# Optimization experiments

Measured on AMD Instinct MI355X. Metric: run time of the kernel, lower is better.

The kernel has to match this reference:

```python
import jax, jax.numpy as jnp
import numpy as np

B, S, D = 2, 2048, 2048
H = 16
DH = D // H  # 128, head dim for q, also the single kv head dim
ROPE_BASE = 10000.0


def _rope_cos_sin(seq_len, dim, dtype):
    inv_freq = 1.0 / (ROPE_BASE ** (jnp.arange(0, dim, 2, dtype=jnp.float32) / dim))
    t = jnp.arange(seq_len, dtype=jnp.float32)
    freqs = jnp.outer(t, inv_freq)            # [S, dim/2]
    emb = jnp.concatenate([freqs, freqs], -1)  # [S, dim]
    return jnp.cos(emb).astype(dtype), jnp.sin(emb).astype(dtype)


def _rotate_half(x):
    x1, x2 = x[..., : x.shape[-1] // 2], x[..., x.shape[-1] // 2 :]
    return jnp.concatenate([-x2, x1], axis=-1)


def setup_inputs() -> dict:
    key = jax.random.key(0)
    ks = jax.random.split(key, 7)
    s = 0.02
    return {
        "x": jax.random.normal(ks[0], (B, S, D), jnp.float32),
        "q_weight": jax.random.normal(ks[1], (H * DH, D), jnp.float32) * s,
        "q_bias": jax.random.normal(ks[2], (H * DH,), jnp.float32) * s,
        "kv_weight": jax.random.normal(ks[3], (2 * DH, D), jnp.float32) * s,
        "kv_bias": jax.random.normal(ks[4], (2 * DH,), jnp.float32) * s,
        "o_weight": jax.random.normal(ks[5], (D, H * DH), jnp.float32) * s,
        "o_bias": jax.random.normal(ks[6], (D,), jnp.float32) * s,
    }


def reference(x, q_weight, q_bias, kv_weight, kv_bias, o_weight, o_bias):
    b, s, d = x.shape
    # fused-style MQA projections (torch F.linear: y = x @ W.T + b)
    q = x @ q_weight.T + q_bias                      # [B,S,H*DH]
    kv = x @ kv_weight.T + kv_bias                   # [B,S,2*DH]
    q = q.reshape(b, s, H, DH)
    k, v = kv[..., :DH], kv[..., DH:]                # [B,S,DH] single kv head

    # rotary embedding (GPT-NeoX / rotate_half style) on q and k
    cos, sin = _rope_cos_sin(s, DH, x.dtype)         # [S,DH]
    q = q * cos[None, :, None, :] + _rotate_half(q) * sin[None, :, None, :]
    k = k * cos[None, :, :] + _rotate_half(k) * sin[None, :, :]

    # causal MQA attention (flash_attn_varlen with full masks == dense causal)
    scale = 1.0 / jnp.sqrt(jnp.asarray(DH, x.dtype))
    scores = jnp.einsum("bqhd,bkd->bhqk", q, k) * scale   # [B,H,S,S]
    causal = jnp.tril(jnp.ones((s, s), bool))
    scores = jnp.where(causal[None, None], scores, jnp.asarray(-1e9, x.dtype))
    probs = jax.nn.softmax(scores, axis=-1)
    attn = jnp.einsum("bhqk,bkd->bqhd", probs, v)         # [B,S,H,DH]

    out = attn.reshape(b, s, H * DH) @ o_weight.T + o_bias
    return out
```

## Files before the change

kernel.cpp:

```cpp
#include <hip/hip_runtime.h>
#include <math.h>

constexpr int Bb  = 2;
constexpr int Ss  = 2048;
constexpr int Dd  = 2048;
constexpr int Hh  = 16;
constexpr int DHd = 128;
constexpr int BS  = Bb * Ss;
constexpr int NQKV = 2304;

typedef __bf16 bf16x8 __attribute__((ext_vector_type(8)));
typedef float  f32x4  __attribute__((ext_vector_type(4)));

static __device__ __forceinline__ unsigned short f2bf(float f) {
  union { float f; unsigned int u; } a; a.f = f;
  unsigned int u = a.u;
  unsigned int r = (u + 0x7fffu + ((u >> 16) & 1u)) >> 16;
  return (unsigned short)r;
}
static __device__ __forceinline__ float bf2f(unsigned short u) {
  union { unsigned int u; float f; } a; a.u = ((unsigned int)u) << 16;
  return a.f;
}
static __device__ __forceinline__ int pk2bf(float lo, float hi) {
  return (int)((unsigned int)f2bf(lo) | ((unsigned int)f2bf(hi) << 16));
}
static __device__ __forceinline__ f32x4 mfma16(bf16x8 a, bf16x8 b, f32x4 c) {
  return __builtin_amdgcn_mfma_f32_16x16x32_bf16(a, b, c, 0, 0, 0);
}

__global__ __launch_bounds__(256) void cast_all(
    const float* __restrict__ qw, const float* __restrict__ kvw,
    const float* __restrict__ ow, const float* __restrict__ x,
    unsigned short* __restrict__ dst)
{
  const int i = blockIdx.x * 256 + threadIdx.x;
  const float* src; int off;
  if (i < 1048576)      { src = qw;  off = 0; }
  else if (i < 1179648) { src = kvw; off = 1048576; }
  else if (i < 2228224) { src = ow;  off = 1179648; }
  else                  { src = x;   off = 2228224; }
  const float4 v = ((const float4*)src)[i - off];
  ushort4 o;
  o.x = f2bf(v.x); o.y = f2bf(v.y); o.z = f2bf(v.z); o.w = f2bf(v.w);
  ((ushort4*)dst)[i] = o;
}

#define TM 128
#define TN 128
#define TK 32

#define GLOAD16(gp, lp)                                                        \
  __builtin_amdgcn_global_load_lds(                                            \
      (const __attribute__((address_space(1))) void*)(gp),                     \
      (__attribute__((address_space(3))) void*)(lp), 16, 0, 0)

template <bool BF16OUT>
__global__ __launch_bounds__(256) void gemm_bt_mfma(
    const unsigned short* __restrict__ A,
    const unsigned short* __restrict__ Bw,
    const float* __restrict__ bias1,
    const float* __restrict__ bias2,
    int nsplit,
    void* __restrict__ Cv,
    int M, int N, int K)
{
  __shared__ unsigned short As[TM * TK];
  __shared__ unsigned short Bs[TN * TK];

  const int tid  = threadIdx.x;
  const int w    = tid >> 6;
  const int lane = tid & 63;
  const int m0   = blockIdx.y * TM;
  const int n0   = blockIdx.x * TN;
  const int wm   = (w >> 1) * 64;
  const int wn   = (w & 1) * 64;

  f32x4 acc[4][4];
#pragma unroll
  for (int i = 0; i < 4; i++)
#pragma unroll
    for (int j = 0; j < 4; j++) acc[i][j] = (f32x4){0.f, 0.f, 0.f, 0.f};

  const int srow = lane >> 2;
  const int scol = (lane & 3) * 8;
  const unsigned short* aG0 = A  + (size_t)(m0 +      w * 16 + srow) * K + scol;
  const unsigned short* aG1 = A  + (size_t)(m0 + 64 + w * 16 + srow) * K + scol;
  const unsigned short* bG0 = Bw + (size_t)(n0 +      w * 16 + srow) * K + scol;
  const unsigned short* bG1 = Bw + (size_t)(n0 + 64 + w * 16 + srow) * K + scol;
  unsigned short* aL0 = &As[(     w * 16) * TK];
  unsigned short* aL1 = &As[(64 + w * 16) * TK];
  unsigned short* bL0 = &Bs[(     w * 16) * TK];
  unsigned short* bL1 = &Bs[(64 + w * 16) * TK];

  const int fr = lane & 15;
  const int fk = (lane >> 4) * 8;

  for (int k0 = 0; k0 < K; k0 += TK) {
    __syncthreads();
    GLOAD16(aG0 + k0, aL0);
    GLOAD16(aG1 + k0, aL1);
    GLOAD16(bG0 + k0, bL0);
    GLOAD16(bG1 + k0, bL1);
    __syncthreads();

    bf16x8 af[4], bfr[4];
#pragma unroll
    for (int i = 0; i < 4; i++)
      af[i] = *(const bf16x8*)&As[(wm + i * 16 + fr) * TK + fk];
#pragma unroll
    for (int j = 0; j < 4; j++)
      bfr[j] = *(const bf16x8*)&Bs[(wn + j * 16 + fr) * TK + fk];
#pragma unroll
    for (int i = 0; i < 4; i++)
#pragma unroll
      for (int j = 0; j < 4; j++)
        acc[i][j] = mfma16(af[i], bfr[j], acc[i][j]);
  }

  const int er = (lane >> 4) * 4;
  const int ec = lane & 15;
#pragma unroll
  for (int j = 0; j < 4; j++) {
    const int col = n0 + wn + j * 16 + ec;
    const float bv = (col < nsplit) ? bias1[col] : bias2[col - nsplit];
#pragma unroll
    for (int i = 0; i < 4; i++) {
      const int rbase = m0 + wm + i * 16 + er;
#pragma unroll
      for (int r = 0; r < 4; r++) {
        const float v = acc[i][j][r] + bv;
        if constexpr (BF16OUT)
          ((unsigned short*)Cv)[(size_t)(rbase + r) * N + col] = f2bf(v);
        else
          ((float*)Cv)[(size_t)(rbase + r) * N + col] = v;
      }
    }
  }
}

__global__ __launch_bounds__(256) void rope_q_bf16(unsigned short* __restrict__ QKV)
{
  const int row = blockIdx.x;
  const int s   = row & (Ss - 1);
  const int t   = threadIdx.x;
  const int h   = t >> 4, p = t & 15;
  unsigned short* base = QKV + (size_t)row * NQKV + h * DHd + p * 4;

  union { ushort4 v; unsigned short a[4]; } lo, hi, olo, ohi;
  lo.v = *(ushort4*)base;
  hi.v = *(ushort4*)(base + 64);
#pragma unroll
  for (int d = 0; d < 4; d++) {
    const int i = p * 4 + d;
    const float invf = exp2f(-(float)i * (13.287712379549449f / 64.0f));
    const float ang = (float)s * invf;
    const float c = cosf(ang), sn = sinf(ang);
    const float l = bf2f(lo.a[d]), hh = bf2f(hi.a[d]);
    olo.a[d] = f2bf(l * c - hh * sn);
    ohi.a[d] = f2bf(hh * c + l * sn);
  }
  *(ushort4*)base        = olo.v;
  *(ushort4*)(base + 64) = ohi.v;
}

__global__ __launch_bounds__(256) void prep_kv(
    const unsigned short* __restrict__ QKV,
    unsigned short* __restrict__ Kb,
    unsigned short* __restrict__ Vt)
{
  __shared__ unsigned short Vtile[64 * 136];

  const int blk = blockIdx.x;
  const int b   = blk >> 5;
  const int s0  = (blk & 31) * 64;
  const int t   = threadIdx.x;

  {
    const int r = t >> 2, p = t & 3;
    const int row = blk * 64 + r;
    const int s = row & (Ss - 1);
    const unsigned short* src = QKV + (size_t)row * NQKV + 2048 + p * 16;
    union { uint4 v[2]; unsigned short a[16]; } lo, hi, ol, oh;
    lo.v[0] = *(const uint4*)src;        lo.v[1] = *(const uint4*)(src + 8);
    hi.v[0] = *(const uint4*)(src + 64); hi.v[1] = *(const uint4*)(src + 72);
#pragma unroll
    for (int e = 0; e < 16; e++) {
      const int i = p * 16 + e;
      const float invf = exp2f(-(float)i * (13.287712379549449f / 64.0f));
      const float ang = (float)s * invf;
      const float c = cosf(ang), sn = sinf(ang);
      const float l = bf2f(lo.a[e]), hh = bf2f(hi.a[e]);
      ol.a[e] = f2bf(l * c - hh * sn);
      oh.a[e] = f2bf(hh * c + l * sn);
    }
    unsigned short* dst = Kb + (size_t)row * 128 + p * 16;
    *(uint4*)dst        = ol.v[0]; *(uint4*)(dst + 8)  = ol.v[1];
    *(uint4*)(dst + 64) = oh.v[0]; *(uint4*)(dst + 72) = oh.v[1];
  }

#pragma unroll
  for (int c = 0; c < 4; c++) {
    const int id = c * 256 + t;
    const int vr = id >> 4, cc = id & 15;
    *(uint4*)&Vtile[vr * 136 + cc * 8] =
        *(const uint4*)(QKV + (size_t)(blk * 64 + vr) * NQKV + 2176 + cc * 8);
  }
  __syncthreads();

  {
    const int d = t >> 1, half = t & 1;
    union { uint4 v[4]; unsigned short a[32]; } val;
#pragma unroll
    for (int kk = 0; kk < 32; kk++)
      val.a[kk] = Vtile[(half * 32 + kk) * 136 + d];
    unsigned short* dst = Vt + ((size_t)(b * 128 + d)) * Ss + s0 + half * 32;
#pragma unroll
    for (int c = 0; c < 4; c++) *(uint4*)(dst + c * 8) = val.v[c];
  }
}

__global__ __launch_bounds__(256, 4) void flash_v7(
    const unsigned short* __restrict__ QKV,
    const unsigned short* __restrict__ Kb,
    const unsigned short* __restrict__ Vt,
    unsigned short* __restrict__ attn)
{
  __shared__ unsigned short Ks[4 * 64 * 32];
  __shared__ unsigned short Vs[2 * 128 * 32];

  const int g   = (int)blockIdx.x;
  const int k4  = g >> 8;
  const int qtp = g & 31;
  const int m   = (g >> 5) & 7;
  const int hb  = m + 8 * k4;
  const int h   = hb & 15;
  const int b   = hb >> 4;
  const int q2  = (k4 & 2) ? ((qtp + 16) & 31) : qtp;
  const int qt  = (k4 & 1) ? (31 - q2) : q2;

  const int q0 = qt * 64;
  const int tid = threadIdx.x;
  const int w = tid >> 6, lane = tid & 63;
  const int lg = lane >> 4, lm = lane & 15;
  const int qrow = q0 + w * 16 + lm;
  const int qrow_hi = q0 + w * 16 + 15;

  bf16x8 qf[4];
  {
    const unsigned short* qp =
        QKV + (size_t)(b * Ss + qrow) * NQKV + h * DHd + lg * 8;
#pragma unroll
    for (int kf = 0; kf < 4; kf++) qf[kf] = *(const bf16x8*)(qp + kf * 32);
  }

  f32x4 ot[8];
#pragma unroll
  for (int dt = 0; dt < 8; dt++) ot[dt] = (f32x4){0.f, 0.f, 0.f, 0.f};
  float lsum = 0.f;

  const float sscale = 0.08838834764831845f * 1.4426950408889634f;

  const int sr  = lane >> 2;
  const int sc8 = (lane & 3) * 8;
  const unsigned short* kg =
      Kb + (size_t)b * Ss * 128 + (size_t)sr * 128 + w * 32 + sc8;
  const unsigned short* vg =
      Vt + (size_t)b * 128 * Ss + (size_t)(w * 32 + sr) * Ss + sc8;
  unsigned short* ksl  = &Ks[w * 2048];
  unsigned short* vsl0 = &Vs[(w * 32) * 32];
  unsigned short* vsl1 = &Vs[4096 + (w * 32) * 32];

  const int addr0 = (2 * (lg & 1)) * 16 + lm;
  const int addr1 = addr0 + 16;
  const bool sel_hi = (lg & 2) != 0;

  auto half32 = [&](int keybase, int tA, const unsigned short* VsP) {
    f32x4 s[2];
    s[0] = (f32x4){0.f, 0.f, 0.f, 0.f};
    s[1] = (f32x4){0.f, 0.f, 0.f, 0.f};
#pragma unroll
    for (int kf = 0; kf < 4; kf++) {
      const bf16x8 k0 = *(const bf16x8*)&Ks[kf * 2048 + ((tA)     * 16 + lm) * 32 + lg * 8];
      const bf16x8 k1 = *(const bf16x8*)&Ks[kf * 2048 + ((tA + 1) * 16 + lm) * 32 + lg * 8];
      s[0] = mfma16(k0, qf[kf], s[0]);
      s[1] = mfma16(k1, qf[kf], s[1]);
    }
    int pk[2][2];
#pragma unroll
    for (int t = 0; t < 2; t++) {
      float p[4];
#pragma unroll
      for (int r = 0; r < 4; r++) {
        const int key = keybase + t * 16 + 4 * lg + r;
        const float ev = exp2f(s[t][r] * sscale);
        p[r] = (key <= qrow) ? ev : 0.f;
        lsum += p[r];
      }
      pk[t][0] = pk2bf(p[0], p[1]);
      pk[t][1] = pk2bf(p[2], p[3]);
    }
    union { int d[4]; bf16x8 v; } pb;
#pragma unroll
    for (int d = 0; d < 4; d++) {
      const int src = (d < 2) ? addr0 : addr1;
      const int v0 = __shfl(pk[0][d & 1], src);
      const int v1 = __shfl(pk[1][d & 1], src);
      pb.d[d] = sel_hi ? v1 : v0;
    }
#pragma unroll
    for (int dt = 0; dt < 8; dt++) {
      const bf16x8 vfrag = *(const bf16x8*)&VsP[(dt * 16 + lm) * 32 + lg * 8];
      ot[dt] = mfma16(vfrag, pb.v, ot[dt]);
    }
  };

  for (int j0 = 0; j0 <= q0; j0 += 64) {
    __syncthreads();
#pragma unroll
    for (int i = 0; i < 4; i++)
      GLOAD16(kg + (size_t)(j0 + i * 16) * 128, ksl + i * 512);
#pragma unroll
    for (int i = 0; i < 2; i++) {
      GLOAD16(vg + (size_t)(i * 16) * Ss + j0,      vsl0 + i * 512);
      GLOAD16(vg + (size_t)(i * 16) * Ss + j0 + 32, vsl1 + i * 512);
    }
    __syncthreads();

    half32(j0, 0, &Vs[0]);
    if (j0 + 32 <= qrow_hi)
      half32(j0 + 32, 2, &Vs[4096]);
  }

  lsum += __shfl_xor(lsum, 16);
  lsum += __shfl_xor(lsum, 32);
  const float inv = 1.0f / lsum;

  unsigned short* dst = attn + (size_t)(b * Ss + qrow) * Dd + h * DHd + lg * 4;
#pragma unroll
  for (int dt = 0; dt < 8; dt++) {
    ushort4 o4;
    o4.x = f2bf(ot[dt][0] * inv);
    o4.y = f2bf(ot[dt][1] * inv);
    o4.z = f2bf(ot[dt][2] * inv);
    o4.w = f2bf(ot[dt][3] * inv);
    *(ushort4*)(dst + dt * 16) = o4;
  }
}

extern "C" void kernel_launch(void* const* d_in, const int* in_sizes, int n_in,
                              void* d_out, int out_size, void* d_ws, size_t ws_size,
                              hipStream_t stream) {
  const float* x   = (const float*)d_in[0];
  const float* qw  = (const float*)d_in[1];
  const float* qb  = (const float*)d_in[2];
  const float* kvw = (const float*)d_in[3];
  const float* kvb = (const float*)d_in[4];
  const float* ow  = (const float*)d_in[5];
  const float* ob  = (const float*)d_in[6];
  float* out = (float*)d_out;

  unsigned short* wsb    = (unsigned short*)d_ws;
  unsigned short* wqkv   = wsb;
  unsigned short* owb    = wsb + 4718592;
  unsigned short* xb     = wsb + 8912896;
  unsigned short* attn_b = xb;
  unsigned short* QKV    = wsb + 17301504;
  unsigned short* Kb     = wsb + 26738688;
  unsigned short* Vt     = wsb + 27262976;

  cast_all<<<16896, 256, 0, stream>>>(qw, kvw, ow, x, wqkv);

  gemm_bt_mfma<true><<<dim3(NQKV / TN, BS / TM), 256, 0, stream>>>(
      xb, wqkv, qb, kvb, 2048, QKV, BS, NQKV, Dd);

  rope_q_bf16<<<BS, 256, 0, stream>>>(QKV);
  prep_kv<<<BS / 64, 256, 0, stream>>>(QKV, Kb, Vt);

  flash_v7<<<1024, 256, 0, stream>>>(QKV, Kb, Vt, attn_b);

  gemm_bt_mfma<false><<<dim3(Dd / TN, BS / TM), 256, 0, stream>>>(
      attn_b, owb, ob, ob, Dd, out, BS, Dd, Dd);
}
```

Before: 324.4 us.

## Fuse Q rotary embedding into flash kernel and XOR-swizzle K/V LDS layout

Removes the standalone rope_q_bf16 kernel and applies the rotary embedding to Q inside the flash attention kernel while its fragments are loaded into registers. This saves one kernel launch and a full read-write pass over the Q portion of the QKV buffer. It also XOR-swizzles the 16-byte chunk position used for the K and V shared-memory stores and reads, aiming to cut LDS bank conflicts. In exchange each flash block recomputes the sin and cos values for its Q rows, which adds transcendental work and register pressure.

```diff
diff --git a/kernel.cpp b/kernel.cpp
--- a/kernel.cpp
+++ b/kernel.cpp
@@ -139,31 +139,6 @@
   }
 }
 
-__global__ __launch_bounds__(256) void rope_q_bf16(unsigned short* __restrict__ QKV)
-{
-  const int row = blockIdx.x;
-  const int s   = row & (Ss - 1);
-  const int t   = threadIdx.x;
-  const int h   = t >> 4, p = t & 15;
-  unsigned short* base = QKV + (size_t)row * NQKV + h * DHd + p * 4;
-
-  union { ushort4 v; unsigned short a[4]; } lo, hi, olo, ohi;
-  lo.v = *(ushort4*)base;
-  hi.v = *(ushort4*)(base + 64);
-#pragma unroll
-  for (int d = 0; d < 4; d++) {
-    const int i = p * 4 + d;
-    const float invf = exp2f(-(float)i * (13.287712379549449f / 64.0f));
-    const float ang = (float)s * invf;
-    const float c = cosf(ang), sn = sinf(ang);
-    const float l = bf2f(lo.a[d]), hh = bf2f(hi.a[d]);
-    olo.a[d] = f2bf(l * c - hh * sn);
-    ohi.a[d] = f2bf(hh * c + l * sn);
-  }
-  *(ushort4*)base        = olo.v;
-  *(ushort4*)(base + 64) = ohi.v;
-}
-
 __global__ __launch_bounds__(256) void prep_kv(
     const unsigned short* __restrict__ QKV,
     unsigned short* __restrict__ Kb,
@@ -220,7 +195,7 @@
   }
 }
 
-__global__ __launch_bounds__(256, 4) void flash_v7(
+__global__ __launch_bounds__(256, 4) void flash_v8(
     const unsigned short* __restrict__ QKV,
     const unsigned short* __restrict__ Kb,
     const unsigned short* __restrict__ Vt,
@@ -246,12 +221,41 @@
   const int qrow = q0 + w * 16 + lm;
   const int qrow_hi = q0 + w * 16 + 15;
 
+  const int klg = lg ^ ((lm >> 1) & 3);
+
   bf16x8 qf[4];
   {
     const unsigned short* qp =
         QKV + (size_t)(b * Ss + qrow) * NQKV + h * DHd + lg * 8;
-#pragma unroll
-    for (int kf = 0; kf < 4; kf++) qf[kf] = *(const bf16x8*)(qp + kf * 32);
+    union U8 { bf16x8 v; unsigned short a[8]; };
+    U8 lo0, lo1, hi0, hi1, ol0, ol1, oh0, oh1;
+    lo0.v = *(const bf16x8*)(qp);
+    lo1.v = *(const bf16x8*)(qp + 32);
+    hi0.v = *(const bf16x8*)(qp + 64);
+    hi1.v = *(const bf16x8*)(qp + 96);
+    const float fs = (float)qrow;
+#pragma unroll
+    for (int j = 0; j < 8; j++) {
+      {
+        const int i = lg * 8 + j;
+        const float invf = exp2f(-(float)i * (13.287712379549449f / 64.0f));
+        const float ang = fs * invf;
+        const float c = cosf(ang), sn = sinf(ang);
+        const float l = bf2f(lo0.a[j]), hh = bf2f(hi0.a[j]);
+        ol0.a[j] = f2bf(l * c - hh * sn);
+        oh0.a[j] = f2bf(hh * c + l * sn);
+      }
+      {
+        const int i = 32 + lg * 8 + j;
+        const float invf = exp2f(-(float)i * (13.287712379549449f / 64.0f));
+        const float ang = fs * invf;
+        const float c = cosf(ang), sn = sinf(ang);
+        const float l = bf2f(lo1.a[j]), hh = bf2f(hi1.a[j]);
+        ol1.a[j] = f2bf(l * c - hh * sn);
+        oh1.a[j] = f2bf(hh * c + l * sn);
+      }
+    }
+    qf[0] = ol0.v; qf[1] = ol1.v; qf[2] = oh0.v; qf[3] = oh1.v;
   }
 
   f32x4 ot[8];
@@ -262,7 +266,7 @@
   const float sscale = 0.08838834764831845f * 1.4426950408889634f;
 
   const int sr  = lane >> 2;
-  const int sc8 = (lane & 3) * 8;
+  const int sc8 = ((lane & 3) ^ ((lane >> 3) & 3)) * 8;
   const unsigned short* kg =
       Kb + (size_t)b * Ss * 128 + (size_t)sr * 128 + w * 32 + sc8;
   const unsigned short* vg =
@@ -281,8 +285,8 @@
     s[1] = (f32x4){0.f, 0.f, 0.f, 0.f};
 #pragma unroll
     for (int kf = 0; kf < 4; kf++) {
-      const bf16x8 k0 = *(const bf16x8*)&Ks[kf * 2048 + ((tA)     * 16 + lm) * 32 + lg * 8];
-      const bf16x8 k1 = *(const bf16x8*)&Ks[kf * 2048 + ((tA + 1) * 16 + lm) * 32 + lg * 8];
+      const bf16x8 k0 = *(const bf16x8*)&Ks[kf * 2048 + ((tA)     * 16 + lm) * 32 + klg * 8];
+      const bf16x8 k1 = *(const bf16x8*)&Ks[kf * 2048 + ((tA + 1) * 16 + lm) * 32 + klg * 8];
       s[0] = mfma16(k0, qf[kf], s[0]);
       s[1] = mfma16(k1, qf[kf], s[1]);
     }
@@ -310,7 +314,7 @@
     }
 #pragma unroll
     for (int dt = 0; dt < 8; dt++) {
-      const bf16x8 vfrag = *(const bf16x8*)&VsP[(dt * 16 + lm) * 32 + lg * 8];
+      const bf16x8 vfrag = *(const bf16x8*)&VsP[(dt * 16 + lm) * 32 + klg * 8];
       ot[dt] = mfma16(vfrag, pb.v, ot[dt]);
     }
   };
@@ -374,10 +378,9 @@
   gemm_bt_mfma<true><<<dim3(NQKV / TN, BS / TM), 256, 0, stream>>>(
       xb, wqkv, qb, kvb, 2048, QKV, BS, NQKV, Dd);
 
-  rope_q_bf16<<<BS, 256, 0, stream>>>(QKV);
   prep_kv<<<BS / 64, 256, 0, stream>>>(QKV, Kb, Vt);
 
-  flash_v7<<<1024, 256, 0, stream>>>(QKV, Kb, Vt, attn_b);
+  flash_v8<<<1024, 256, 0, stream>>>(QKV, Kb, Vt, attn_b);
 
   gemm_bt_mfma<false><<<dim3(Dd / TN, BS / TM), 256, 0, stream>>>(
       attn_b, owb, ob, ob, Dd, out, BS, Dd, Dd);
```

Measured after the change: 319.5 us. No clear change (-1.5%).
